# Optimization experiments

Hardware: AMD Instinct MI355X
Metric: run time of the kernel (lower is better)

The kernel has to match this reference:

```python
import jax, jax.numpy as jnp
import numpy as np

B, S, H = 1, 2048, 2880
NH, NKV, HD = 64, 8, 64
WIN = 128
ROPE_BASE = 10000.0


def setup_inputs() -> dict:
    key = jax.random.key(0)
    ks = jax.random.split(key, 8)

    def lin(k, fi, fo):
        return (jax.random.normal(k, (fi, fo), jnp.float32) / np.sqrt(fi)).astype(jnp.float32)

    hidden_states = jax.random.normal(ks[0], (B, S, H), jnp.float32)
    Wq = lin(ks[1], H, NH * HD)
    Wk = lin(ks[2], H, NKV * HD)
    Wv = lin(ks[3], H, NKV * HD)
    Wo = lin(ks[4], NH * HD, H)
    bq = jnp.zeros((NH * HD,), jnp.float32)
    bk = jnp.zeros((NKV * HD,), jnp.float32)
    bv = jnp.zeros((NKV * HD,), jnp.float32)
    bo = jnp.zeros((H,), jnp.float32)
    sinks = jax.random.normal(ks[5], (NH,), jnp.float32) * 0.5

    # RoPE tables, shape [B, S, HD] (rotate_half convention: halves duplicated)
    pos = jnp.arange(S, dtype=jnp.float32)
    inv_freq = 1.0 / (ROPE_BASE ** (jnp.arange(0, HD, 2, dtype=jnp.float32) / HD))
    freqs = pos[:, None] * inv_freq[None, :]          # [S, HD/2]
    emb = jnp.concatenate([freqs, freqs], axis=-1)    # [S, HD]
    cos = jnp.broadcast_to(jnp.cos(emb)[None], (B, S, HD))
    sin = jnp.broadcast_to(jnp.sin(emb)[None], (B, S, HD))

    return dict(hidden_states=hidden_states, cos=cos, sin=sin,
                Wq=Wq, bq=bq, Wk=Wk, bk=bk, Wv=Wv, bv=bv, Wo=Wo, bo=bo,
                sinks=sinks, window=WIN)


def _rotate_half(x):
    x1, x2 = jnp.split(x, 2, axis=-1)
    return jnp.concatenate([-x2, x1], axis=-1)


def reference(hidden_states, cos, sin, Wq, bq, Wk, bk, Wv, bv, Wo, bo, sinks, window):
    b, s, _ = hidden_states.shape
    nh = sinks.shape[0]
    hd = Wq.shape[1] // nh
    nkv = Wk.shape[1] // hd
    scale = hd ** -0.5

    q = (hidden_states @ Wq + bq).reshape(b, s, nh, hd)
    k = (hidden_states @ Wk + bk).reshape(b, s, nkv, hd)
    v = (hidden_states @ Wv + bv).reshape(b, s, nkv, hd)

    c = cos[:, :, None, :]  # [b, s, 1, hd]
    sn = sin[:, :, None, :]
    q = q * c + _rotate_half(q) * sn
    k = k * c + _rotate_half(k) * sn

    # GQA: expand kv heads to query heads
    g = nh // nkv
    k_rep = jnp.repeat(k, g, axis=2)  # [b, s, nh, hd]
    v_rep = jnp.repeat(v, g, axis=2)

    scores = jnp.einsum('bqhd,bkhd->bhqk', q, k_rep) * scale  # [b, nh, s, s]

    # causal sliding-window mask
    qi = jnp.arange(s)[:, None]
    ki = jnp.arange(s)[None, :]
    allowed = (qi >= ki) & (qi - ki < window)
    neg = jnp.finfo(scores.dtype).min
    scores = jnp.where(allowed[None, None], scores, neg)

    # virtual sink column at kv index s: score replaced by learned per-head bias
    sink_col = jnp.broadcast_to(sinks[None, :, None, None], (b, nh, s, 1))
    scores = jnp.concatenate([scores, sink_col], axis=-1)  # [b, nh, s, s+1]

    probs = jax.nn.softmax(scores, axis=-1)
    # sink value vector is zeros, so only real columns contribute
    out = jnp.einsum('bhqk,bkhd->bqhd', probs[..., :s], v_rep)
    out = out.reshape(b, s, nh * hd) @ Wo + bo
    return out
```

## Files before the change

kernel.cpp:

```cpp
#include <hip/hip_runtime.h>
#include <stdint.h>
#include <stddef.h>

typedef unsigned short u16;
typedef unsigned int u32;
typedef float f32x4 __attribute__((ext_vector_type(4)));
typedef __bf16 bf16x8 __attribute__((ext_vector_type(8)));
typedef uint32_t u32x4 __attribute__((ext_vector_type(4)));
typedef uint32_t u32x2 __attribute__((ext_vector_type(2)));

#define DEVINL static __device__ __forceinline__
#define VMW(n) asm volatile("s_waitcnt vmcnt(" #n ")" ::: "memory")
#define LGK0() asm volatile("s_waitcnt lgkmcnt(0)" ::: "memory")
#define SB0() __builtin_amdgcn_sched_barrier(0)

DEVINL u16 f2bf(float f) {
  union { float f; u32 u; } x; x.f = f;
  u32 r = (x.u + 0x7fffu + ((x.u >> 16) & 1u)) >> 16;
  return (u16)r;
}
DEVINL float bflo(u32 x) { union { u32 u; float f; } t; t.u = x << 16; return t.f; }
DEVINL float bfhi(u32 x) { union { u32 u; float f; } t; t.u = x & 0xffff0000u; return t.f; }

DEVINL void gl_lds16(const u16* g, u16* l) {
  __builtin_amdgcn_global_load_lds(
      (const __attribute__((address_space(1))) u32*)(const void*)g,
      (__attribute__((address_space(3))) u32*)(void*)l, 16, 0, 0);
}

DEVINL f32x4 mfma16(bf16x8 a, bf16x8 b, f32x4 c) {
  return __builtin_amdgcn_mfma_f32_16x16x32_bf16(a, b, c, 0, 0, 0);
}

__global__ void k_cvt(const float* __restrict__ src, u16* __restrict__ dst, int n4) {
  int i = blockIdx.x * 256 + threadIdx.x;
  if (i >= n4) return;
  f32x4 v = ((const f32x4*)src)[i];
  u32x2 o;
  o[0] = (u32)f2bf(v[0]) | ((u32)f2bf(v[1]) << 16);
  o[1] = (u32)f2bf(v[2]) | ((u32)f2bf(v[3]) << 16);
  ((u32x2*)dst)[i] = o;
}

__global__ __launch_bounds__(256) void k_tcvt2(const float* __restrict__ src,
                                               u16* __restrict__ dst, int R, int C) {
  __shared__ float t[64][65];
  const int tid = threadIdx.x;
  const int r0 = blockIdx.y * 64, c0 = blockIdx.x * 64;
  {
    const int rr = tid >> 2, cg = (tid & 3) * 16;
    const float* s = src + (size_t)(r0 + rr) * C + c0 + cg;
#pragma unroll
    for (int i = 0; i < 4; ++i) {
      f32x4 v = *(const f32x4*)(s + 4 * i);
      t[rr][cg + 4 * i + 0] = v[0];
      t[rr][cg + 4 * i + 1] = v[1];
      t[rr][cg + 4 * i + 2] = v[2];
      t[rr][cg + 4 * i + 3] = v[3];
    }
  }
  __syncthreads();
  {
    const int rg = tid & 7, cb = tid >> 3;
#pragma unroll
    for (int it = 0; it < 2; ++it) {
      const int c = cb + it * 32;
      float v[8];
#pragma unroll
      for (int i = 0; i < 8; ++i) v[i] = t[rg * 8 + i][c];
      u32x4 o;
#pragma unroll
      for (int j = 0; j < 4; ++j)
        o[j] = (u32)f2bf(v[2 * j]) | ((u32)f2bf(v[2 * j + 1]) << 16);
      *(u32x4*)(dst + (size_t)(c0 + c) * R + r0 + rg * 8) = o;
    }
  }
}

__global__ __launch_bounds__(256, 2) void k_gemmq(
    const u16* __restrict__ A, const u16* __restrict__ Bgl, u16* __restrict__ Cout,
    const float* __restrict__ pb0, const float* __restrict__ pb1, const float* __restrict__ pb2)
{
  constexpr int K = 2880, NT = 45, LDC = 5120;
  __shared__ u16 Asm[2][128 * 64];
  __shared__ u16 Bsm[2][160 * 64];

  const int bid = blockIdx.x;
  const int swz = (bid & 7) * 64 + (bid >> 3);
  const int bx = swz >> 4, by = swz & 15;
  const int m0 = by * 128, n0 = bx * 160;

  const int tid = threadIdx.x;
  const int w = tid >> 6, lane = tid & 63;
  const int l15 = lane & 15, lg = lane >> 4;
  const int wr = w >> 1, wc = w & 1;

  const u16* Ag = A + (size_t)m0 * K;
  const u16* Bg = Bgl + (size_t)n0 * K;

  auto ld1 = [&](const u16* s, u16* d, int slot) {
    int row = slot >> 3, c = slot & 7;
    gl_lds16(s + (size_t)row * K + ((c ^ (row & 7)) << 3), d + row * 64 + c * 8);
  };
  auto stApart = [&](int tg, int part) {
    u16* d = Asm[tg & 1];
    const u16* s = Ag + tg * 64;
    ld1(s, d, part * 256 + tid);
    ld1(s, d, part * 256 + 512 + tid);
  };
  auto stBa = [&](int tg) {
    u16* d = Bsm[tg & 1];
    const u16* s = Bg + tg * 64;
    ld1(s, d, tid);
    ld1(s, d, 640 + tid);
  };
  auto stBb = [&](int tg) {
    u16* d = Bsm[tg & 1];
    const u16* s = Bg + tg * 64;
    ld1(s, d, 256 + tid);
    ld1(s, d, (tid < 128) ? (512 + tid) : (768 + tid));
    ld1(s, d, 1024 + tid);
  };

  const int ra = wr * 64 + l15;
  const int rb = wc * 80 + l15;
  const int x0 = (lg ^ (l15 & 7)) << 3;
  const int x1 = x0 ^ 32;

  f32x4 acc[4][5] = {};
  bf16x8 af[2][2], bfr[5][2];

  stBa(0); stBb(0); stApart(0, 0); stApart(0, 1);
  VMW(2);
  __builtin_amdgcn_s_barrier();
  SB0();

  for (int t = 0; t < NT; ++t) {
    const u16* Ab = Asm[t & 1];
    const u16* Bb_ = Bsm[t & 1];
    const bool st = (t + 1 < NT);
#pragma unroll
    for (int m = 0; m < 2; ++m) {
      af[m][0] = *(const bf16x8*)&Ab[(ra + m * 16) * 64 + x0];
      af[m][1] = *(const bf16x8*)&Ab[(ra + m * 16) * 64 + x1];
    }
#pragma unroll
    for (int n = 0; n < 2; ++n) {
      bfr[n][0] = *(const bf16x8*)&Bb_[(rb + n * 16) * 64 + x0];
      bfr[n][1] = *(const bf16x8*)&Bb_[(rb + n * 16) * 64 + x1];
    }
    if (st) stBa(t + 1);
    LGK0(); SB0();
    __builtin_amdgcn_s_setprio(1);
#pragma unroll
    for (int kk = 0; kk < 2; ++kk)
#pragma unroll
      for (int m = 0; m < 2; ++m)
#pragma unroll
        for (int n = 0; n < 2; ++n)
          acc[m][n] = mfma16(af[m][kk], bfr[n][kk], acc[m][n]);
    __builtin_amdgcn_s_setprio(0);
#pragma unroll
    for (int n = 2; n < 5; ++n) {
      bfr[n][0] = *(const bf16x8*)&Bb_[(rb + n * 16) * 64 + x0];
      bfr[n][1] = *(const bf16x8*)&Bb_[(rb + n * 16) * 64 + x1];
    }
    if (st) stBb(t + 1);
    LGK0(); SB0();
    __builtin_amdgcn_s_setprio(1);
#pragma unroll
    for (int kk = 0; kk < 2; ++kk)
#pragma unroll
      for (int m = 0; m < 2; ++m)
#pragma unroll
        for (int n = 2; n < 5; ++n)
          acc[m][n] = mfma16(af[m][kk], bfr[n][kk], acc[m][n]);
    __builtin_amdgcn_s_setprio(0);
    if (st) { VMW(5); } else { VMW(0); }
    __builtin_amdgcn_s_barrier();
    SB0();
#pragma unroll
    for (int m = 0; m < 2; ++m) {
      af[m][0] = *(const bf16x8*)&Ab[(ra + 32 + m * 16) * 64 + x0];
      af[m][1] = *(const bf16x8*)&Ab[(ra + 32 + m * 16) * 64 + x1];
    }
    if (st) stApart(t + 1, 0);
    LGK0(); SB0();
    __builtin_amdgcn_s_setprio(1);
#pragma unroll
    for (int kk = 0; kk < 2; ++kk)
#pragma unroll
      for (int m = 0; m < 2; ++m)
#pragma unroll
        for (int n = 0; n < 2; ++n)
          acc[2 + m][n] = mfma16(af[m][kk], bfr[n][kk], acc[2 + m][n]);
    __builtin_amdgcn_s_setprio(0);
    if (st) stApart(t + 1, 1);
    __builtin_amdgcn_s_setprio(1);
#pragma unroll
    for (int kk = 0; kk < 2; ++kk)
#pragma unroll
      for (int m = 0; m < 2; ++m)
#pragma unroll
        for (int n = 2; n < 5; ++n)
          acc[2 + m][n] = mfma16(af[m][kk], bfr[n][kk], acc[2 + m][n]);
    __builtin_amdgcn_s_setprio(0);
    VMW(2);
    __builtin_amdgcn_s_barrier();
    SB0();
  }

#pragma unroll
  for (int m2 = 0; m2 < 4; ++m2)
#pragma unroll
    for (int n = 0; n < 5; ++n) {
      int col = n0 + wc * 80 + n * 16 + l15;
      float bias = (col < 4096) ? pb0[col] : (col < 4608) ? pb1[col - 4096] : pb2[col - 4608];
#pragma unroll
      for (int q = 0; q < 4; ++q) {
        int row = m0 + wr * 64 + m2 * 16 + lg * 4 + q;
        Cout[(size_t)row * LDC + col] = f2bf(acc[m2][n][q] + bias);
      }
    }
}

__global__ __launch_bounds__(256, 2) void k_gemmo(
    const u16* __restrict__ A, const u16* __restrict__ Bgl, float* __restrict__ Cout,
    const float* __restrict__ pb0)
{
  constexpr int K = 4096, NT = 64, LDC = 2880;
  __shared__ u16 Asm[2][128 * 64];
  __shared__ u16 Bsm[2][96 * 64];

  const int bid = blockIdx.x;
  const int swz = (bid & 7) * 60 + (bid >> 3);
  const int bx = swz / 16, by = swz & 15;
  const int m0 = by * 128, n0 = bx * 96;

  const int tid = threadIdx.x;
  const int w = tid >> 6, lane = tid & 63;
  const int l15 = lane & 15, lg = lane >> 4;
  const int wr = w >> 1, wc = w & 1;

  const u16* Ag = A + (size_t)m0 * K;
  const u16* Bg = Bgl + (size_t)n0 * K;

  auto ld1 = [&](const u16* s, u16* d, int slot) {
    int row = slot >> 3, c = slot & 7;
    gl_lds16(s + (size_t)row * K + ((c ^ (row & 7)) << 3), d + row * 64 + c * 8);
  };
  auto stApart = [&](int tg, int part) {
    u16* d = Asm[tg & 1];
    const u16* s = Ag + tg * 64;
    ld1(s, d, part * 256 + tid);
    ld1(s, d, part * 256 + 512 + tid);
  };
  auto stB = [&](int tg) {
    u16* d = Bsm[tg & 1];
    const u16* s = Bg + tg * 64;
    ld1(s, d, tid);
    ld1(s, d, 256 + tid);
    ld1(s, d, 512 + tid);
  };

  const int ra = wr * 64 + l15;
  const int rb = wc * 48 + l15;
  const int x0 = (lg ^ (l15 & 7)) << 3;
  const int x1 = x0 ^ 32;

  f32x4 acc[4][3] = {};
  bf16x8 af[2][2], bfr[3][2];

  stB(0); stApart(0, 0); stApart(0, 1);
  VMW(2);
  __builtin_amdgcn_s_barrier();
  SB0();

  for (int t = 0; t < NT; ++t) {
    const u16* Ab = Asm[t & 1];
    const u16* Bb_ = Bsm[t & 1];
    const bool st = (t + 1 < NT);
#pragma unroll
    for (int m = 0; m < 2; ++m) {
      af[m][0] = *(const bf16x8*)&Ab[(ra + m * 16) * 64 + x0];
      af[m][1] = *(const bf16x8*)&Ab[(ra + m * 16) * 64 + x1];
    }
#pragma unroll
    for (int n = 0; n < 3; ++n) {
      bfr[n][0] = *(const bf16x8*)&Bb_[(rb + n * 16) * 64 + x0];
      bfr[n][1] = *(const bf16x8*)&Bb_[(rb + n * 16) * 64 + x1];
    }
    if (st) { stB(t + 1); stApart(t + 1, 0); }
    LGK0(); SB0();
    __builtin_amdgcn_s_setprio(1);
#pragma unroll
    for (int kk = 0; kk < 2; ++kk)
#pragma unroll
      for (int m = 0; m < 2; ++m)
#pragma unroll
        for (int n = 0; n < 3; ++n)
          acc[m][n] = mfma16(af[m][kk], bfr[n][kk], acc[m][n]);
    __builtin_amdgcn_s_setprio(0);
    if (st) { VMW(5); } else { VMW(0); }
    __builtin_amdgcn_s_barrier();
    SB0();
#pragma unroll
    for (int m = 0; m < 2; ++m) {
      af[m][0] = *(const bf16x8*)&Ab[(ra + 32 + m * 16) * 64 + x0];
      af[m][1] = *(const bf16x8*)&Ab[(ra + 32 + m * 16) * 64 + x1];
    }
    if (st) stApart(t + 1, 1);
    LGK0(); SB0();
    __builtin_amdgcn_s_setprio(1);
#pragma unroll
    for (int kk = 0; kk < 2; ++kk)
#pragma unroll
      for (int m = 0; m < 2; ++m)
#pragma unroll
        for (int n = 0; n < 3; ++n)
          acc[2 + m][n] = mfma16(af[m][kk], bfr[n][kk], acc[2 + m][n]);
    __builtin_amdgcn_s_setprio(0);
    VMW(2);
    __builtin_amdgcn_s_barrier();
    SB0();
  }

#pragma unroll
  for (int m2 = 0; m2 < 4; ++m2)
#pragma unroll
    for (int n = 0; n < 3; ++n) {
      int col = n0 + wc * 48 + n * 16 + l15;
      float bias = pb0[col];
#pragma unroll
      for (int q = 0; q < 4; ++q) {
        int row = m0 + wr * 64 + m2 * 16 + lg * 4 + q;
        Cout[(size_t)row * LDC + col] = acc[m2][n][q] + bias;
      }
    }
}

__global__ void k_rope(u16* __restrict__ qkv, const float* __restrict__ cosb,
                       const float* __restrict__ sinb) {
  int idx = blockIdx.x * 256 + threadIdx.x;
  if (idx >= 2048 * 72 * 4) return;
  int oct = idx & 3;
  int h = (idx >> 2) % 72;
  int s = idx / 288;
  u16* p1 = qkv + (size_t)s * 5120 + h * 64 + oct * 8;
  u16* p2 = p1 + 32;
  const float* pc = cosb + (size_t)s * 64 + oct * 8;
  const float* ps = sinb + (size_t)s * 64 + oct * 8;
  u32x4 a = *(const u32x4*)p1;
  u32x4 b = *(const u32x4*)p2;
  f32x4 c0 = *(const f32x4*)pc, c1 = *(const f32x4*)(pc + 4);
  f32x4 s0 = *(const f32x4*)ps, s1 = *(const f32x4*)(ps + 4);
  float C[8] = {c0[0], c0[1], c0[2], c0[3], c1[0], c1[1], c1[2], c1[3]};
  float Sn[8] = {s0[0], s0[1], s0[2], s0[3], s1[0], s1[1], s1[2], s1[3]};
  u32x4 ra, rb;
#pragma unroll
  for (int i = 0; i < 4; ++i) {
    float x1l = bflo(a[i]), x1h = bfhi(a[i]);
    float x2l = bflo(b[i]), x2h = bfhi(b[i]);
    float o1l = x1l * C[2 * i] - x2l * Sn[2 * i];
    float o1h = x1h * C[2 * i + 1] - x2h * Sn[2 * i + 1];
    float o2l = x2l * C[2 * i] + x1l * Sn[2 * i];
    float o2h = x2h * C[2 * i + 1] + x1h * Sn[2 * i + 1];
    ra[i] = (u32)f2bf(o1l) | ((u32)f2bf(o1h) << 16);
    rb[i] = (u32)f2bf(o2l) | ((u32)f2bf(o2h) << 16);
  }
  *(u32x4*)p1 = ra;
  *(u32x4*)p2 = rb;
}

__global__ __launch_bounds__(512, 1) void k_attn(
    const u16* __restrict__ qkv, const float* __restrict__ sinks, u16* __restrict__ aout)
{
  __shared__ u16 Kl[192 * 64];
  __shared__ u16 Vt[64 * 200];
  __shared__ u16 Pl[8][2][16][40];

  const int qt = blockIdx.x * 64;
  const int kv = blockIdx.y;
  const int tid = threadIdx.x;
  const int w = tid >> 6, lane = tid & 63;
  const int l15 = lane & 15, lg = lane >> 4;

  for (int idx = tid; idx < 192 * 8; idx += 512) {
    int row = idx >> 3, ch = idx & 7;
    int key = qt - 128 + row;
    u32x4 val = {0, 0, 0, 0};
    if (key >= 0) val = *(const u32x4*)(qkv + (size_t)key * 5120 + 4096 + kv * 64 + ch * 8);
    *(u32x4*)((char*)Kl + row * 128 + ((ch * 16) ^ ((row & 7) << 4))) = val;
  }
  for (int idx = tid; idx < 192 * 8; idx += 512) {
    int row = idx >> 3, ch = idx & 7;
    int key = qt - 128 + row;
    u32x4 val = {0, 0, 0, 0};
    if (key >= 0) val = *(const u32x4*)(qkv + (size_t)key * 5120 + 4608 + kv * 64 + ch * 8);
    const u16* pv16 = (const u16*)&val;
#pragma unroll
    for (int j = 0; j < 8; ++j) Vt[(ch * 8 + j) * 200 + row] = pv16[j];
  }
  __syncthreads();

  const int h = kv * 8 + w;
  const float sink = sinks[h];

  for (int qs = 0; qs < 2; ++qs) {
    const int qb = qt + qs * 32;
    bf16x8 qf[2][2];
#pragma unroll
    for (int rt = 0; rt < 2; ++rt)
#pragma unroll
      for (int ks = 0; ks < 2; ++ks)
        qf[rt][ks] = *(const bf16x8*)(qkv + (size_t)(qb + rt * 16 + l15) * 5120 + h * 64 + ks * 32 + lg * 8);

    f32x4 S[2][5][2];
#pragma unroll
    for (int kb = 0; kb < 5; ++kb)
#pragma unroll
      for (int hh = 0; hh < 2; ++hh) {
        int krow = qs * 32 + kb * 32 + hh * 16 + l15;
        int sw = (krow & 7) << 4;
        bf16x8 kf0 = *(const bf16x8*)((const char*)Kl + krow * 128 + ((lg * 16) ^ sw));
        bf16x8 kf1 = *(const bf16x8*)((const char*)Kl + krow * 128 + ((64 + lg * 16) ^ sw));
#pragma unroll
        for (int rt = 0; rt < 2; ++rt) {
          f32x4 a = {0.f, 0.f, 0.f, 0.f};
          a = mfma16(qf[rt][0], kf0, a);
          a = mfma16(qf[rt][1], kf1, a);
          S[rt][kb][hh] = a;
        }
      }

    float inv_s[2][4];
#pragma unroll
    for (int rt = 0; rt < 2; ++rt)
#pragma unroll
      for (int r = 0; r < 4; ++r) {
        int q_abs = qb + rt * 16 + lg * 4 + r;
        float m = -1e30f;
#pragma unroll
        for (int kb = 0; kb < 5; ++kb)
#pragma unroll
          for (int hh = 0; hh < 2; ++hh) {
            int k_abs = qb - 128 + kb * 32 + hh * 16 + l15;
            float v = S[rt][kb][hh][r] * 0.125f;
            bool ok = (k_abs >= 0) && (k_abs <= q_abs) && (q_abs - k_abs < 128);
            v = ok ? v : -1e30f;
            S[rt][kb][hh][r] = v;
            m = fmaxf(m, v);
          }
        m = fmaxf(m, __shfl_xor(m, 1, 64));
        m = fmaxf(m, __shfl_xor(m, 2, 64));
        m = fmaxf(m, __shfl_xor(m, 4, 64));
        m = fmaxf(m, __shfl_xor(m, 8, 64));
        m = fmaxf(m, sink);
        float sum = 0.f;
#pragma unroll
        for (int kb = 0; kb < 5; ++kb)
#pragma unroll
          for (int hh = 0; hh < 2; ++hh) {
            float p = __expf(S[rt][kb][hh][r] - m);
            S[rt][kb][hh][r] = p;
            sum += p;
          }
        sum += __shfl_xor(sum, 1, 64);
        sum += __shfl_xor(sum, 2, 64);
        sum += __shfl_xor(sum, 4, 64);
        sum += __shfl_xor(sum, 8, 64);
        inv_s[rt][r] = 1.0f / (sum + __expf(sink - m));
      }

    f32x4 pv[2][4] = {};
#pragma unroll
    for (int kb = 0; kb < 5; ++kb) {
      asm volatile("s_waitcnt lgkmcnt(0)" ::: "memory");
#pragma unroll
      for (int rt = 0; rt < 2; ++rt)
#pragma unroll
        for (int hh = 0; hh < 2; ++hh)
#pragma unroll
          for (int r = 0; r < 4; ++r)
            Pl[w][rt][lg * 4 + r][hh * 16 + l15] = f2bf(S[rt][kb][hh][r] * inv_s[rt][r]);
      asm volatile("s_waitcnt lgkmcnt(0)" ::: "memory");
      __builtin_amdgcn_sched_barrier(0);
      bf16x8 a0 = *(const bf16x8*)&Pl[w][0][l15][lg * 8];
      bf16x8 a1 = *(const bf16x8*)&Pl[w][1][l15][lg * 8];
#pragma unroll
      for (int nt = 0; nt < 4; ++nt) {
        bf16x8 vf = *(const bf16x8*)&Vt[(nt * 16 + l15) * 200 + qs * 32 + kb * 32 + lg * 8];
        pv[0][nt] = mfma16(a0, vf, pv[0][nt]);
        pv[1][nt] = mfma16(a1, vf, pv[1][nt]);
      }
    }

#pragma unroll
    for (int rt = 0; rt < 2; ++rt)
#pragma unroll
      for (int nt = 0; nt < 4; ++nt)
#pragma unroll
        for (int r = 0; r < 4; ++r)
          aout[(size_t)(qb + rt * 16 + lg * 4 + r) * 4096 + h * 64 + nt * 16 + l15] =
              f2bf(pv[rt][nt][r]);
  }
}

extern "C" void kernel_launch(void* const* d_in, const int* in_sizes, int n_in,
                              void* d_out, int out_size, void* d_ws, size_t ws_size,
                              hipStream_t stream) {
  const float* hs    = (const float*)d_in[0];
  const float* cosb  = (const float*)d_in[1];
  const float* sinb  = (const float*)d_in[2];
  const float* Wq    = (const float*)d_in[3];
  const float* bq    = (const float*)d_in[4];
  const float* Wk    = (const float*)d_in[5];
  const float* bk    = (const float*)d_in[6];
  const float* Wv    = (const float*)d_in[7];
  const float* bv    = (const float*)d_in[8];
  const float* Wo    = (const float*)d_in[9];
  const float* bo    = (const float*)d_in[10];
  const float* sinks = (const float*)d_in[11];

  char* ws = (char*)d_ws;
  u16* hsb   = (u16*)ws;  ws += (size_t)2048 * 2880 * 2;
  u16* WqkvT = (u16*)ws;  ws += (size_t)5120 * 2880 * 2;
  u16* WoT   = (u16*)ws;  ws += (size_t)2880 * 4096 * 2;
  u16* QKV   = (u16*)ws;  ws += (size_t)2048 * 5120 * 2;
  u16* AOut  = (u16*)ws;  ws += (size_t)2048 * 4096 * 2;

  k_cvt<<<5760, 256, 0, stream>>>(hs, hsb, 1474560);
  k_tcvt2<<<dim3(4096 / 64, 2880 / 64), 256, 0, stream>>>(Wq, WqkvT, 2880, 4096);
  k_tcvt2<<<dim3(512 / 64, 2880 / 64), 256, 0, stream>>>(Wk, WqkvT + (size_t)4096 * 2880, 2880, 512);
  k_tcvt2<<<dim3(512 / 64, 2880 / 64), 256, 0, stream>>>(Wv, WqkvT + (size_t)4608 * 2880, 2880, 512);
  k_tcvt2<<<dim3(2880 / 64, 4096 / 64), 256, 0, stream>>>(Wo, WoT, 4096, 2880);

  k_gemmq<<<512, 256, 0, stream>>>(hsb, WqkvT, QKV, bq, bk, bv);

  k_rope<<<2304, 256, 0, stream>>>(QKV, cosb, sinb);

  k_attn<<<dim3(32, 8), 512, 0, stream>>>(QKV, sinks, AOut);

  k_gemmo<<<480, 256, 0, stream>>>(AOut, WoT, (float*)d_out, bo);
}
```

Measured before the change: 182.2 us.

## Load GEMM A operand directly into registers and triple-buffer B in LDS

Both projection GEMMs stop staging the A tile through LDS. Each wave now loads its A fragments straight from global memory into registers, double-buffered across tiles, while B is staged through a three-deep LDS ring with a two-tile prefetch distance. The aim is to cut LDS traffic and the barriers tied to A, and to hide global latency better. In exchange the kernels need more registers, which could hurt occupancy, and the direct A loads are uncoalesced 16-byte reads per lane, whose latency now depends on the vmcnt accounting being right.

```diff
diff --git a/kernel.cpp b/kernel.cpp
--- a/kernel.cpp
+++ b/kernel.cpp
@@ -82,8 +82,7 @@
     const float* __restrict__ pb0, const float* __restrict__ pb1, const float* __restrict__ pb2)
 {
   constexpr int K = 2880, NT = 45, LDC = 5120;
-  __shared__ u16 Asm[2][128 * 64];
-  __shared__ u16 Bsm[2][160 * 64];
+  __shared__ u16 Bsm[3][160 * 64];
 
   const int bid = blockIdx.x;
   const int swz = (bid & 7) * 64 + (bid >> 3);
@@ -95,120 +94,105 @@
   const int l15 = lane & 15, lg = lane >> 4;
   const int wr = w >> 1, wc = w & 1;
 
-  const u16* Ag = A + (size_t)m0 * K;
   const u16* Bg = Bgl + (size_t)n0 * K;
+  const u16* pA = A + (size_t)(m0 + wr * 64 + l15) * K + lg * 8;
 
   auto ld1 = [&](const u16* s, u16* d, int slot) {
     int row = slot >> 3, c = slot & 7;
     gl_lds16(s + (size_t)row * K + ((c ^ (row & 7)) << 3), d + row * 64 + c * 8);
   };
-  auto stApart = [&](int tg, int part) {
-    u16* d = Asm[tg & 1];
-    const u16* s = Ag + tg * 64;
-    ld1(s, d, part * 256 + tid);
-    ld1(s, d, part * 256 + 512 + tid);
-  };
   auto stBa = [&](int tg) {
-    u16* d = Bsm[tg & 1];
+    u16* d = Bsm[tg % 3];
     const u16* s = Bg + tg * 64;
-    ld1(s, d, tid);
-    ld1(s, d, 640 + tid);
+    ld1(s, d, tid); ld1(s, d, 640 + tid);
   };
   auto stBb = [&](int tg) {
-    u16* d = Bsm[tg & 1];
+    u16* d = Bsm[tg % 3];
     const u16* s = Bg + tg * 64;
     ld1(s, d, 256 + tid);
     ld1(s, d, (tid < 128) ? (512 + tid) : (768 + tid));
     ld1(s, d, 1024 + tid);
   };
-
-  const int ra = wr * 64 + l15;
+  auto ldA = [&](int tg, int mh, bf16x8* dst) {
+    const u16* p = pA + tg * 64;
+#pragma unroll
+    for (int m = 0; m < 2; ++m) {
+      dst[m * 2 + 0] = *(const bf16x8*)(p + (size_t)(mh * 32 + m * 16) * K);
+      dst[m * 2 + 1] = *(const bf16x8*)(p + (size_t)(mh * 32 + m * 16) * K + 32);
+    }
+  };
+
   const int rb = wc * 80 + l15;
   const int x0 = (lg ^ (l15 & 7)) << 3;
   const int x1 = x0 ^ 32;
 
   f32x4 acc[4][5] = {};
-  bf16x8 af[2][2], bfr[5][2];
-
-  stBa(0); stBb(0); stApart(0, 0); stApart(0, 1);
-  VMW(2);
+  bf16x8 afA[8], afB[8];
+
+  stBa(0); stBb(0);
+  SB0();
+  ldA(0, 0, afA + 0); ldA(0, 1, afA + 4);
+  SB0();
+  stBa(1); stBb(1);
+  VMW(13);
   __builtin_amdgcn_s_barrier();
   SB0();
 
-  for (int t = 0; t < NT; ++t) {
-    const u16* Ab = Asm[t & 1];
-    const u16* Bb_ = Bsm[t & 1];
-    const bool st = (t + 1 < NT);
-#pragma unroll
-    for (int m = 0; m < 2; ++m) {
-      af[m][0] = *(const bf16x8*)&Ab[(ra + m * 16) * 64 + x0];
-      af[m][1] = *(const bf16x8*)&Ab[(ra + m * 16) * 64 + x1];
-    }
-#pragma unroll
-    for (int n = 0; n < 2; ++n) {
-      bfr[n][0] = *(const bf16x8*)&Bb_[(rb + n * 16) * 64 + x0];
-      bfr[n][1] = *(const bf16x8*)&Bb_[(rb + n * 16) * 64 + x1];
-    }
-    if (st) stBa(t + 1);
-    LGK0(); SB0();
-    __builtin_amdgcn_s_setprio(1);
-#pragma unroll
-    for (int kk = 0; kk < 2; ++kk)
-#pragma unroll
-      for (int m = 0; m < 2; ++m)
-#pragma unroll
-        for (int n = 0; n < 2; ++n)
-          acc[m][n] = mfma16(af[m][kk], bfr[n][kk], acc[m][n]);
-    __builtin_amdgcn_s_setprio(0);
-#pragma unroll
-    for (int n = 2; n < 5; ++n) {
-      bfr[n][0] = *(const bf16x8*)&Bb_[(rb + n * 16) * 64 + x0];
-      bfr[n][1] = *(const bf16x8*)&Bb_[(rb + n * 16) * 64 + x1];
-    }
-    if (st) stBb(t + 1);
-    LGK0(); SB0();
-    __builtin_amdgcn_s_setprio(1);
-#pragma unroll
-    for (int kk = 0; kk < 2; ++kk)
-#pragma unroll
-      for (int m = 0; m < 2; ++m)
-#pragma unroll
-        for (int n = 2; n < 5; ++n)
-          acc[m][n] = mfma16(af[m][kk], bfr[n][kk], acc[m][n]);
-    __builtin_amdgcn_s_setprio(0);
-    if (st) { VMW(5); } else { VMW(0); }
-    __builtin_amdgcn_s_barrier();
-    SB0();
-#pragma unroll
-    for (int m = 0; m < 2; ++m) {
-      af[m][0] = *(const bf16x8*)&Ab[(ra + 32 + m * 16) * 64 + x0];
-      af[m][1] = *(const bf16x8*)&Ab[(ra + 32 + m * 16) * 64 + x1];
-    }
-    if (st) stApart(t + 1, 0);
-    LGK0(); SB0();
-    __builtin_amdgcn_s_setprio(1);
-#pragma unroll
-    for (int kk = 0; kk < 2; ++kk)
-#pragma unroll
-      for (int m = 0; m < 2; ++m)
-#pragma unroll
-        for (int n = 0; n < 2; ++n)
-          acc[2 + m][n] = mfma16(af[m][kk], bfr[n][kk], acc[2 + m][n]);
-    __builtin_amdgcn_s_setprio(0);
-    if (st) stApart(t + 1, 1);
-    __builtin_amdgcn_s_setprio(1);
-#pragma unroll
-    for (int kk = 0; kk < 2; ++kk)
-#pragma unroll
-      for (int m = 0; m < 2; ++m)
-#pragma unroll
-        for (int n = 2; n < 5; ++n)
-          acc[2 + m][n] = mfma16(af[m][kk], bfr[n][kk], acc[2 + m][n]);
-    __builtin_amdgcn_s_setprio(0);
-    VMW(2);
-    __builtin_amdgcn_s_barrier();
-    SB0();
-  }
+  auto tile = [&](int t, bf16x8 (&cur)[8], bf16x8 (&nxt)[8]) {
+    const u16* Bb_ = Bsm[t % 3];
+    const bool s2 = (t + 2 < NT), s1 = (t + 1 < NT);
+    {
+      bf16x8 b0[3][2];
+#pragma unroll
+      for (int n = 0; n < 3; ++n) {
+        b0[n][0] = *(const bf16x8*)&Bb_[(rb + n * 16) * 64 + x0];
+        b0[n][1] = *(const bf16x8*)&Bb_[(rb + n * 16) * 64 + x1];
+      }
+      if (s1) ldA(t + 1, 0, nxt + 0);
+      SB0();
+      if (s2) stBa(t + 2);
+      SB0();
+      LGK0(); SB0();
+      __builtin_amdgcn_s_setprio(1);
+#pragma unroll
+      for (int kk = 0; kk < 2; ++kk)
+#pragma unroll
+        for (int m = 0; m < 4; ++m)
+#pragma unroll
+          for (int n = 0; n < 3; ++n)
+            acc[m][n] = mfma16(cur[m * 2 + kk], b0[n][kk], acc[m][n]);
+      __builtin_amdgcn_s_setprio(0);
+    }
+    {
+      bf16x8 b1[2][2];
+#pragma unroll
+      for (int n = 0; n < 2; ++n) {
+        b1[n][0] = *(const bf16x8*)&Bb_[(rb + 48 + n * 16) * 64 + x0];
+        b1[n][1] = *(const bf16x8*)&Bb_[(rb + 48 + n * 16) * 64 + x1];
+      }
+      if (s1) ldA(t + 1, 1, nxt + 4);
+      SB0();
+      if (s2) stBb(t + 2);
+      SB0();
+      LGK0(); SB0();
+      __builtin_amdgcn_s_setprio(1);
+#pragma unroll
+      for (int kk = 0; kk < 2; ++kk)
+#pragma unroll
+        for (int m = 0; m < 4; ++m)
+#pragma unroll
+          for (int n = 0; n < 2; ++n)
+            acc[m][3 + n] = mfma16(cur[m * 2 + kk], b1[n][kk], acc[m][3 + n]);
+      __builtin_amdgcn_s_setprio(0);
+      if (s2) { VMW(13); } else if (s1) { VMW(8); } else { VMW(0); }
+      __builtin_amdgcn_s_barrier();
+      SB0();
+    }
+  };
+
+  int t = 0;
+  for (; t + 1 < NT; t += 2) { tile(t, afA, afB); tile(t + 1, afB, afA); }
+  tile(NT - 1, afA, afB);
 
 #pragma unroll
   for (int m2 = 0; m2 < 4; ++m2)
@@ -229,8 +213,7 @@
     const float* __restrict__ pb0)
 {
   constexpr int K = 4096, NT = 64, LDC = 2880;
-  __shared__ u16 Asm[2][128 * 64];
-  __shared__ u16 Bsm[2][96 * 64];
+  __shared__ u16 Bsm[3][96 * 64];
 
   const int bid = blockIdx.x;
   const int swz = (bid & 7) * 60 + (bid >> 3);
@@ -242,88 +225,96 @@
   const int l15 = lane & 15, lg = lane >> 4;
   const int wr = w >> 1, wc = w & 1;
 
-  const u16* Ag = A + (size_t)m0 * K;
   const u16* Bg = Bgl + (size_t)n0 * K;
+  const u16* pA = A + (size_t)(m0 + wr * 64 + l15) * K + lg * 8;
 
   auto ld1 = [&](const u16* s, u16* d, int slot) {
     int row = slot >> 3, c = slot & 7;
     gl_lds16(s + (size_t)row * K + ((c ^ (row & 7)) << 3), d + row * 64 + c * 8);
   };
-  auto stApart = [&](int tg, int part) {
-    u16* d = Asm[tg & 1];
-    const u16* s = Ag + tg * 64;
-    ld1(s, d, part * 256 + tid);
-    ld1(s, d, part * 256 + 512 + tid);
-  };
-  auto stB = [&](int tg) {
-    u16* d = Bsm[tg & 1];
+  auto stBa = [&](int tg) {
+    u16* d = Bsm[tg % 3];
     const u16* s = Bg + tg * 64;
-    ld1(s, d, tid);
-    ld1(s, d, 256 + tid);
+    ld1(s, d, tid); ld1(s, d, 256 + tid);
+  };
+  auto stBb = [&](int tg) {
+    u16* d = Bsm[tg % 3];
+    const u16* s = Bg + tg * 64;
     ld1(s, d, 512 + tid);
   };
-
-  const int ra = wr * 64 + l15;
+  auto ldA = [&](int tg, int mh, bf16x8* dst) {
+    const u16* p = pA + tg * 64;
+#pragma unroll
+    for (int m = 0; m < 2; ++m) {
+      dst[m * 2 + 0] = *(const bf16x8*)(p + (size_t)(mh * 32 + m * 16) * K);
+      dst[m * 2 + 1] = *(const bf16x8*)(p + (size_t)(mh * 32 + m * 16) * K + 32);
+    }
+  };
+
   const int rb = wc * 48 + l15;
   const int x0 = (lg ^ (l15 & 7)) << 3;
   const int x1 = x0 ^ 32;
 
   f32x4 acc[4][3] = {};
-  bf16x8 af[2][2], bfr[3][2];
-
-  stB(0); stApart(0, 0); stApart(0, 1);
-  VMW(2);
+  bf16x8 afA[8], afB[8];
+
+  stBa(0); stBb(0);
+  SB0();
+  ldA(0, 0, afA + 0); ldA(0, 1, afA + 4);
+  SB0();
+  stBa(1); stBb(1);
+  VMW(11);
   __builtin_amdgcn_s_barrier();
   SB0();
 
-  for (int t = 0; t < NT; ++t) {
-    const u16* Ab = Asm[t & 1];
-    const u16* Bb_ = Bsm[t & 1];
-    const bool st = (t + 1 < NT);
-#pragma unroll
-    for (int m = 0; m < 2; ++m) {
-      af[m][0] = *(const bf16x8*)&Ab[(ra + m * 16) * 64 + x0];
-      af[m][1] = *(const bf16x8*)&Ab[(ra + m * 16) * 64 + x1];
-    }
-#pragma unroll
-    for (int n = 0; n < 3; ++n) {
-      bfr[n][0] = *(const bf16x8*)&Bb_[(rb + n * 16) * 64 + x0];
-      bfr[n][1] = *(const bf16x8*)&Bb_[(rb + n * 16) * 64 + x1];
-    }
-    if (st) { stB(t + 1); stApart(t + 1, 0); }
-    LGK0(); SB0();
-    __builtin_amdgcn_s_setprio(1);
-#pragma unroll
-    for (int kk = 0; kk < 2; ++kk)
-#pragma unroll
-      for (int m = 0; m < 2; ++m)
-#pragma unroll
-        for (int n = 0; n < 3; ++n)
-          acc[m][n] = mfma16(af[m][kk], bfr[n][kk], acc[m][n]);
-    __builtin_amdgcn_s_setprio(0);
-    if (st) { VMW(5); } else { VMW(0); }
-    __builtin_amdgcn_s_barrier();
-    SB0();
-#pragma unroll
-    for (int m = 0; m < 2; ++m) {
-      af[m][0] = *(const bf16x8*)&Ab[(ra + 32 + m * 16) * 64 + x0];
-      af[m][1] = *(const bf16x8*)&Ab[(ra + 32 + m * 16) * 64 + x1];
-    }
-    if (st) stApart(t + 1, 1);
-    LGK0(); SB0();
-    __builtin_amdgcn_s_setprio(1);
-#pragma unroll
-    for (int kk = 0; kk < 2; ++kk)
-#pragma unroll
-      for (int m = 0; m < 2; ++m)
-#pragma unroll
-        for (int n = 0; n < 3; ++n)
-          acc[2 + m][n] = mfma16(af[m][kk], bfr[n][kk], acc[2 + m][n]);
-    __builtin_amdgcn_s_setprio(0);
-    VMW(2);
-    __builtin_amdgcn_s_barrier();
-    SB0();
-  }
+  auto tile = [&](int t, bf16x8 (&cur)[8], bf16x8 (&nxt)[8]) {
+    const u16* Bb_ = Bsm[t % 3];
+    const bool s2 = (t + 2 < NT), s1 = (t + 1 < NT);
+    {
+      bf16x8 b0[2][2];
+#pragma unroll
+      for (int n = 0; n < 2; ++n) {
+        b0[n][0] = *(const bf16x8*)&Bb_[(rb + n * 16) * 64 + x0];
+        b0[n][1] = *(const bf16x8*)&Bb_[(rb + n * 16) * 64 + x1];
+      }
+      if (s1) ldA(t + 1, 0, nxt + 0);
+      SB0();
+      if (s2) stBa(t + 2);
+      SB0();
+      LGK0(); SB0();
+      __builtin_amdgcn_s_setprio(1);
+#pragma unroll
+      for (int kk = 0; kk < 2; ++kk)
+#pragma unroll
+        for (int m = 0; m < 4; ++m)
+#pragma unroll
+          for (int n = 0; n < 2; ++n)
+            acc[m][n] = mfma16(cur[m * 2 + kk], b0[n][kk], acc[m][n]);
+      __builtin_amdgcn_s_setprio(0);
+    }
+    {
+      bf16x8 b1[2];
+      b1[0] = *(const bf16x8*)&Bb_[(rb + 32) * 64 + x0];
+      b1[1] = *(const bf16x8*)&Bb_[(rb + 32) * 64 + x1];
+      if (s1) ldA(t + 1, 1, nxt + 4);
+      SB0();
+      if (s2) stBb(t + 2);
+      SB0();
+      LGK0(); SB0();
+      __builtin_amdgcn_s_setprio(1);
+#pragma unroll
+      for (int kk = 0; kk < 2; ++kk)
+#pragma unroll
+        for (int m = 0; m < 4; ++m)
+          acc[m][2] = mfma16(cur[m * 2 + kk], b1[kk], acc[m][2]);
+      __builtin_amdgcn_s_setprio(0);
+      if (s2) { VMW(11); } else if (s1) { VMW(8); } else { VMW(0); }
+      __builtin_amdgcn_s_barrier();
+      SB0();
+    }
+  };
+
+  for (int t = 0; t + 1 < NT; t += 2) { tile(t, afA, afB); tile(t + 1, afB, afA); }
 
 #pragma unroll
   for (int m2 = 0; m2 < 4; ++m2)
```

Result: slower. 301.2 us (+65.3%).

## Fuse RoPE into attention loads and merge conversion kernels into one launch

Applied to the files above, without the earlier changes.

The separate RoPE pass over QKV is removed. Rotary embedding is now applied on the fly inside the attention kernel, both when K tiles are staged into LDS and when Q fragments are loaded. Separately, the hidden-state conversion and four weight transpose-conversion launches are merged into one k_pre kernel that dispatches on block index. This removes a full read-modify-write of QKV and several launch gaps, at the cost of redundant RoPE work on K rows that overlap between neighbouring attention blocks and extra cos/sin loads inside attention.

```diff
diff --git a/kernel.cpp b/kernel.cpp
--- a/kernel.cpp
+++ b/kernel.cpp
@@ -32,21 +32,51 @@
   return __builtin_amdgcn_mfma_f32_16x16x32_bf16(a, b, c, 0, 0, 0);
 }
 
-__global__ void k_cvt(const float* __restrict__ src, u16* __restrict__ dst, int n4) {
-  int i = blockIdx.x * 256 + threadIdx.x;
-  if (i >= n4) return;
-  f32x4 v = ((const f32x4*)src)[i];
-  u32x2 o;
-  o[0] = (u32)f2bf(v[0]) | ((u32)f2bf(v[1]) << 16);
-  o[1] = (u32)f2bf(v[2]) | ((u32)f2bf(v[3]) << 16);
-  ((u32x2*)dst)[i] = o;
-}
-
-__global__ __launch_bounds__(256) void k_tcvt2(const float* __restrict__ src,
-                                               u16* __restrict__ dst, int R, int C) {
+DEVINL void rope8(u32x4& v1, u32x4& v2, const float* pc, const float* ps) {
+  f32x4 c0 = *(const f32x4*)pc, c1 = *(const f32x4*)(pc + 4);
+  f32x4 s0 = *(const f32x4*)ps, s1 = *(const f32x4*)(ps + 4);
+  float C[8] = {c0[0], c0[1], c0[2], c0[3], c1[0], c1[1], c1[2], c1[3]};
+  float Sn[8] = {s0[0], s0[1], s0[2], s0[3], s1[0], s1[1], s1[2], s1[3]};
+  u32x4 r1, r2;
+#pragma unroll
+  for (int i = 0; i < 4; ++i) {
+    float x1l = bflo(v1[i]), x1h = bfhi(v1[i]);
+    float x2l = bflo(v2[i]), x2h = bfhi(v2[i]);
+    float o1l = x1l * C[2 * i] - x2l * Sn[2 * i];
+    float o1h = x1h * C[2 * i + 1] - x2h * Sn[2 * i + 1];
+    float o2l = x2l * C[2 * i] + x1l * Sn[2 * i];
+    float o2h = x2h * C[2 * i + 1] + x1h * Sn[2 * i + 1];
+    r1[i] = (u32)f2bf(o1l) | ((u32)f2bf(o1h) << 16);
+    r2[i] = (u32)f2bf(o2l) | ((u32)f2bf(o2h) << 16);
+  }
+  v1 = r1; v2 = r2;
+}
+
+__global__ __launch_bounds__(256) void k_pre(
+    const float* __restrict__ hs, u16* __restrict__ hsb,
+    const float* __restrict__ Wq, const float* __restrict__ Wk,
+    const float* __restrict__ Wv, const float* __restrict__ Wo,
+    u16* __restrict__ WqkvT, u16* __restrict__ WoT)
+{
   __shared__ float t[64][65];
+  int id = blockIdx.x;
   const int tid = threadIdx.x;
-  const int r0 = blockIdx.y * 64, c0 = blockIdx.x * 64;
+  if (id < 5760) {
+    int i = id * 256 + tid;
+    f32x4 v = ((const f32x4*)hs)[i];
+    u32x2 o;
+    o[0] = (u32)f2bf(v[0]) | ((u32)f2bf(v[1]) << 16);
+    o[1] = (u32)f2bf(v[2]) | ((u32)f2bf(v[3]) << 16);
+    ((u32x2*)hsb)[i] = o;
+    return;
+  }
+  id -= 5760;
+  const float* src; u16* dst; int R, C, bx, by;
+  if (id < 2880)       { src = Wq; dst = WqkvT;                         R = 2880; C = 4096; bx = id & 63; by = id >> 6; }
+  else if (id < 3240)  { id -= 2880; src = Wk; dst = WqkvT + (size_t)4096 * 2880; R = 2880; C = 512;  bx = id & 7;  by = id >> 3; }
+  else if (id < 3600)  { id -= 3240; src = Wv; dst = WqkvT + (size_t)4608 * 2880; R = 2880; C = 512;  bx = id & 7;  by = id >> 3; }
+  else                 { id -= 3600; src = Wo; dst = WoT;               R = 4096; C = 2880; bx = id % 45; by = id / 45; }
+  const int r0 = by * 64, c0 = bx * 64;
   {
     const int rr = tid >> 2, cg = (tid & 3) * 16;
     const float* s = src + (size_t)(r0 + rr) * C + c0 + cg;
@@ -339,41 +369,10 @@
     }
 }
 
-__global__ void k_rope(u16* __restrict__ qkv, const float* __restrict__ cosb,
-                       const float* __restrict__ sinb) {
-  int idx = blockIdx.x * 256 + threadIdx.x;
-  if (idx >= 2048 * 72 * 4) return;
-  int oct = idx & 3;
-  int h = (idx >> 2) % 72;
-  int s = idx / 288;
-  u16* p1 = qkv + (size_t)s * 5120 + h * 64 + oct * 8;
-  u16* p2 = p1 + 32;
-  const float* pc = cosb + (size_t)s * 64 + oct * 8;
-  const float* ps = sinb + (size_t)s * 64 + oct * 8;
-  u32x4 a = *(const u32x4*)p1;
-  u32x4 b = *(const u32x4*)p2;
-  f32x4 c0 = *(const f32x4*)pc, c1 = *(const f32x4*)(pc + 4);
-  f32x4 s0 = *(const f32x4*)ps, s1 = *(const f32x4*)(ps + 4);
-  float C[8] = {c0[0], c0[1], c0[2], c0[3], c1[0], c1[1], c1[2], c1[3]};
-  float Sn[8] = {s0[0], s0[1], s0[2], s0[3], s1[0], s1[1], s1[2], s1[3]};
-  u32x4 ra, rb;
-#pragma unroll
-  for (int i = 0; i < 4; ++i) {
-    float x1l = bflo(a[i]), x1h = bfhi(a[i]);
-    float x2l = bflo(b[i]), x2h = bfhi(b[i]);
-    float o1l = x1l * C[2 * i] - x2l * Sn[2 * i];
-    float o1h = x1h * C[2 * i + 1] - x2h * Sn[2 * i + 1];
-    float o2l = x2l * C[2 * i] + x1l * Sn[2 * i];
-    float o2h = x2h * C[2 * i + 1] + x1h * Sn[2 * i + 1];
-    ra[i] = (u32)f2bf(o1l) | ((u32)f2bf(o1h) << 16);
-    rb[i] = (u32)f2bf(o2l) | ((u32)f2bf(o2h) << 16);
-  }
-  *(u32x4*)p1 = ra;
-  *(u32x4*)p2 = rb;
-}
-
 __global__ __launch_bounds__(512, 1) void k_attn(
-    const u16* __restrict__ qkv, const float* __restrict__ sinks, u16* __restrict__ aout)
+    const u16* __restrict__ qkv, const float* __restrict__ sinks,
+    const float* __restrict__ cosb, const float* __restrict__ sinb,
+    u16* __restrict__ aout)
 {
   __shared__ u16 Kl[192 * 64];
   __shared__ u16 Vt[64 * 200];
@@ -385,12 +384,19 @@
   const int w = tid >> 6, lane = tid & 63;
   const int l15 = lane & 15, lg = lane >> 4;
 
-  for (int idx = tid; idx < 192 * 8; idx += 512) {
-    int row = idx >> 3, ch = idx & 7;
+  for (int idx = tid; idx < 192 * 4; idx += 512) {
+    int row = idx >> 2, ch = idx & 3;
     int key = qt - 128 + row;
-    u32x4 val = {0, 0, 0, 0};
-    if (key >= 0) val = *(const u32x4*)(qkv + (size_t)key * 5120 + 4096 + kv * 64 + ch * 8);
-    *(u32x4*)((char*)Kl + row * 128 + ((ch * 16) ^ ((row & 7) << 4))) = val;
+    u32x4 v1 = {0, 0, 0, 0}, v2 = {0, 0, 0, 0};
+    if (key >= 0) {
+      const u16* p = qkv + (size_t)key * 5120 + 4096 + kv * 64 + ch * 8;
+      v1 = *(const u32x4*)p;
+      v2 = *(const u32x4*)(p + 32);
+      rope8(v1, v2, cosb + (size_t)key * 64 + ch * 8, sinb + (size_t)key * 64 + ch * 8);
+    }
+    int sw = (row & 7) << 4;
+    *(u32x4*)((char*)Kl + row * 128 + ((ch * 16) ^ sw)) = v1;
+    *(u32x4*)((char*)Kl + row * 128 + (((ch + 4) * 16) ^ sw)) = v2;
   }
   for (int idx = tid; idx < 192 * 8; idx += 512) {
     int row = idx >> 3, ch = idx & 7;
@@ -410,10 +416,16 @@
     const int qb = qt + qs * 32;
     bf16x8 qf[2][2];
 #pragma unroll
-    for (int rt = 0; rt < 2; ++rt)
-#pragma unroll
-      for (int ks = 0; ks < 2; ++ks)
-        qf[rt][ks] = *(const bf16x8*)(qkv + (size_t)(qb + rt * 16 + l15) * 5120 + h * 64 + ks * 32 + lg * 8);
+    for (int rt = 0; rt < 2; ++rt) {
+      const int qrow = qb + rt * 16 + l15;
+      const u16* p = qkv + (size_t)qrow * 5120 + h * 64 + lg * 8;
+      union { u32x4 u; bf16x8 v; } a, b;
+      a.u = *(const u32x4*)p;
+      b.u = *(const u32x4*)(p + 32);
+      rope8(a.u, b.u, cosb + (size_t)qrow * 64 + lg * 8, sinb + (size_t)qrow * 64 + lg * 8);
+      qf[rt][0] = a.v;
+      qf[rt][1] = b.v;
+    }
 
     f32x4 S[2][5][2];
 #pragma unroll
@@ -529,17 +541,11 @@
   u16* QKV   = (u16*)ws;  ws += (size_t)2048 * 5120 * 2;
   u16* AOut  = (u16*)ws;  ws += (size_t)2048 * 4096 * 2;
 
-  k_cvt<<<5760, 256, 0, stream>>>(hs, hsb, 1474560);
-  k_tcvt2<<<dim3(4096 / 64, 2880 / 64), 256, 0, stream>>>(Wq, WqkvT, 2880, 4096);
-  k_tcvt2<<<dim3(512 / 64, 2880 / 64), 256, 0, stream>>>(Wk, WqkvT + (size_t)4096 * 2880, 2880, 512);
-  k_tcvt2<<<dim3(512 / 64, 2880 / 64), 256, 0, stream>>>(Wv, WqkvT + (size_t)4608 * 2880, 2880, 512);
-  k_tcvt2<<<dim3(2880 / 64, 4096 / 64), 256, 0, stream>>>(Wo, WoT, 4096, 2880);
+  k_pre<<<12240, 256, 0, stream>>>(hs, hsb, Wq, Wk, Wv, Wo, WqkvT, WoT);
 
   k_gemmq<<<512, 256, 0, stream>>>(hsb, WqkvT, QKV, bq, bk, bv);
 
-  k_rope<<<2304, 256, 0, stream>>>(QKV, cosb, sinb);
-
-  k_attn<<<dim3(32, 8), 512, 0, stream>>>(QKV, sinks, AOut);
+  k_attn<<<dim3(32, 8), 512, 0, stream>>>(QKV, sinks, cosb, sinb, AOut);
 
   k_gemmo<<<480, 256, 0, stream>>>(AOut, WoT, (float*)d_out, bo);
 }
```

Result: faster. 167.8 us (-7.9%).
